# Performance work log

Hardware: AMD Instinct MI355X
Metric: run time of the kernel (lower is better)

The kernel has to match this reference:

```python
import jax, jax.numpy as jnp
import numpy as np

N = 100000
E = 3200000
F_IN, H1, H2, C = 512, 32, 16, 11


def setup_inputs() -> dict:
    key = jax.random.key(0)
    ks = jax.random.split(key, 8)
    x = jax.random.normal(ks[0], (N, F_IN), dtype=jnp.float32)
    edge_index = jax.random.randint(ks[1], (2, E), 0, N, dtype=jnp.int64)
    def glorot(k, fan_in, fan_out):
        lim = np.sqrt(6.0 / (fan_in + fan_out)).astype(np.float32)
        return jax.random.uniform(k, (fan_in, fan_out), jnp.float32, -lim, lim)
    return {
        "x": x,
        "edge_index": edge_index,
        "W1": glorot(ks[2], F_IN, H1), "b1": jnp.zeros((H1,), jnp.float32),
        "W2": glorot(ks[3], H1, H2),   "b2": jnp.zeros((H2,), jnp.float32),
        "W3": glorot(ks[4], H2, C),    "b3": jnp.zeros((C,), jnp.float32),
    }


def _gcn_conv(x, W, b, src, dst, deg_inv_sqrt):
    # GCNConv: D^{-1/2}(A+I)D^{-1/2} X W + b, self-loops handled analytically.
    h = x @ W                                   # [N, out]
    norm = deg_inv_sqrt[src] * deg_inv_sqrt[dst]  # [E]
    msg = h[src] * norm[:, None]                # gather + scale
    agg = jax.ops.segment_sum(msg, dst, num_segments=x.shape[0])
    agg = agg + h * (deg_inv_sqrt ** 2)[:, None]  # self-loop term
    return agg + b


def reference(x, edge_index, W1, b1, W2, b2, W3, b3):
    src, dst = edge_index[0], edge_index[1]
    n = x.shape[0]
    # degree with self-loops, counted on destination (PyG convention)
    deg = jax.ops.segment_sum(jnp.ones((dst.shape[0],), x.dtype), dst, num_segments=n) + 1.0
    deg_inv_sqrt = jax.lax.rsqrt(deg)
    h = jax.nn.relu(_gcn_conv(x, W1, b1, src, dst, deg_inv_sqrt))
    # F.dropout(training=self.training) is identity in eval mode
    h = jax.nn.relu(_gcn_conv(h, W2, b2, src, dst, deg_inv_sqrt))
    h = _gcn_conv(h, W3, b3, src, dst, deg_inv_sqrt)
    return jax.nn.log_softmax(h, axis=1)
```

## Files before the change

### kernel.cpp

```cpp
#include <hip/hip_runtime.h>
#include <hip/hip_bf16.h>

static __device__ __forceinline__ unsigned short f2bf(float f) {
    unsigned u = __float_as_uint(f);
    unsigned r = (u + 0x7FFF + ((u >> 16) & 1)) >> 16;
    return (unsigned short)r;
}
static __device__ __forceinline__ float bf2f(unsigned short h) {
    return __uint_as_float(((unsigned)h) << 16);
}
static __device__ __forceinline__ float bflo(unsigned v) { return __uint_as_float(v << 16); }
static __device__ __forceinline__ float bfhi(unsigned v) { return __uint_as_float(v & 0xFFFF0000u); }
static __device__ __forceinline__ unsigned pack2bf(float a, float b) {
    __hip_bfloat162 h2 = __float22bfloat162_rn(float2{a, b});
    union { __hip_bfloat162 h; unsigned u; } cv;
    cv.h = h2;
    return cv.u;
}

typedef __attribute__((ext_vector_type(8))) short bf16x8;
typedef __attribute__((ext_vector_type(8))) unsigned short u16x8;
typedef __attribute__((ext_vector_type(4))) float f32x4;

#define BKT_SHIFT 7
#define BKT_NODES 128
#define CHUNK 16384

__global__ __launch_bounds__(512) void hist_k(const int* __restrict__ dst, int* __restrict__ histG,
                                              int B, int NB, int E) {
    __shared__ int hist[1024];
    int tid = threadIdx.x;
    for (int i = tid; i < NB; i += 512) hist[i] = 0;
    __syncthreads();
    int base = blockIdx.x * CHUNK;
    for (int i = tid; i < CHUNK; i += 512) {
        int e = base + i;
        if (e >= E) break;
        atomicAdd(&hist[dst[e] >> BKT_SHIFT], 1);
    }
    __syncthreads();
    for (int i = tid; i < NB; i += 512) histG[(size_t)i * B + blockIdx.x] = hist[i];
}

__global__ __launch_bounds__(512) void scatter_k(const int* __restrict__ src, const int* __restrict__ dst,
                                                 const int* __restrict__ scanG, const int* __restrict__ blksum,
                                                 int* __restrict__ pairs, int B, int NB, int E) {
    __shared__ int sbase[1024];
    __shared__ int scnt[1024];
    int tid = threadIdx.x;
    for (int i = tid; i < NB; i += 512) {
        size_t idx = (size_t)i * B + blockIdx.x;
        sbase[i] = scanG[idx] + blksum[idx >> 11];
        scnt[i] = 0;
    }
    __syncthreads();
    int base = blockIdx.x * CHUNK;
    for (int i = tid; i < CHUNK; i += 512) {
        int e = base + i;
        if (e >= E) break;
        int d = dst[e], s = src[e];
        int b = d >> BKT_SHIFT;
        int r = atomicAdd(&scnt[b], 1);
        pairs[sbase[b] + r] = (s << BKT_SHIFT) | (d & (BKT_NODES - 1));
    }
}

#define SCAN_VPT 8
#define SCAN_ELEMS 2048

__global__ __launch_bounds__(256) void scan1(const int* __restrict__ in, int* __restrict__ out,
                                             int* __restrict__ blksum, int n) {
    __shared__ int sh[256];
    int base = blockIdx.x * SCAN_ELEMS + threadIdx.x * SCAN_VPT;
    int v[SCAN_VPT];
    int sum = 0;
    #pragma unroll
    for (int j = 0; j < SCAN_VPT; ++j) {
        v[j] = (base + j < n) ? in[base + j] : 0;
        sum += v[j];
    }
    sh[threadIdx.x] = sum;
    __syncthreads();
    for (int off = 1; off < 256; off <<= 1) {
        int t = (threadIdx.x >= off) ? sh[threadIdx.x - off] : 0;
        __syncthreads();
        sh[threadIdx.x] += t;
        __syncthreads();
    }
    if (threadIdx.x == 255) blksum[blockIdx.x] = sh[255];
    int run = sh[threadIdx.x] - sum;
    #pragma unroll
    for (int j = 0; j < SCAN_VPT; ++j) {
        if (base + j < n) out[base + j] = run;
        run += v[j];
    }
}

__global__ __launch_bounds__(256) void scan2(int* __restrict__ blksum, int nb) {
    __shared__ int sh[256];
    int t = threadIdx.x;
    int v = (t < nb) ? blksum[t] : 0;
    sh[t] = v;
    __syncthreads();
    for (int off = 1; off < 256; off <<= 1) {
        int u = (t >= off) ? sh[t - off] : 0;
        __syncthreads();
        sh[t] += u;
        __syncthreads();
    }
    if (t < nb) blksum[t] = sh[t] - v;
}

__global__ __launch_bounds__(256) void wconv(const float* __restrict__ W, unsigned short* __restrict__ W1T) {
    int gidx = blockIdx.x * 256 + threadIdx.x;
    if (gidx < 32 * 512) {
        int c = gidx >> 9, k = gidx & 511;
        W1T[gidx] = f2bf(W[(size_t)k * 32 + c]);
    }
}

#define SORT_CAP 8192

__global__ __launch_bounds__(512) void sort_bucket(const int* __restrict__ pairs,
        const int* __restrict__ scanG, const int* __restrict__ blksum, int B, int NB,
        int* __restrict__ csr_src, int* __restrict__ node_start,
        int* __restrict__ cnt, float* __restrict__ dis, int n, int E) {
    __shared__ int keys[SORT_CAP];
    __shared__ int lcnt[BKT_NODES];
    __shared__ int lscan[BKT_NODES];
    __shared__ int lfill[BKT_NODES];
    int bkt = blockIdx.x, tid = threadIdx.x;
    size_t idx0 = (size_t)bkt * B;
    int e0 = scanG[idx0] + blksum[idx0 >> 11];
    int e1 = E;
    if (bkt + 1 < NB) {
        size_t idx1 = (size_t)(bkt + 1) * B;
        e1 = scanG[idx1] + blksum[idx1 >> 11];
    }
    int m = e1 - e0;
    if (tid < BKT_NODES) { lcnt[tid] = 0; lfill[tid] = 0; }
    __syncthreads();
    for (int i = tid; i < m; i += 512) {
        int k = pairs[e0 + i];
        if (i < SORT_CAP) keys[i] = k;
        atomicAdd(&lcnt[k & (BKT_NODES - 1)], 1);
    }
    __syncthreads();
    if (tid < 64) {
        int c0 = lcnt[2 * tid], c1 = lcnt[2 * tid + 1];
        int s = c0 + c1;
        #pragma unroll
        for (int off = 1; off < 64; off <<= 1) {
            int t = __shfl_up(s, off);
            if (tid >= off) s += t;
        }
        lscan[2 * tid]     = s - c1 - c0;
        lscan[2 * tid + 1] = s - c1;
    }
    __syncthreads();
    int nb0 = bkt << BKT_SHIFT;
    if (tid < BKT_NODES && nb0 + tid < n) {
        int deg = lcnt[tid];
        node_start[nb0 + tid] = e0 + lscan[tid];
        cnt[nb0 + tid] = deg;
        dis[nb0 + tid] = rsqrtf((float)deg + 1.0f);
    }
    for (int i = tid; i < m; i += 512) {
        int k = (i < SORT_CAP) ? keys[i] : pairs[e0 + i];
        int d = k & (BKT_NODES - 1);
        int pos = lscan[d] + atomicAdd(&lfill[d], 1);
        csr_src[e0 + pos] = k >> BKT_SHIFT;
    }
}


__global__ __launch_bounds__(256) void gemm1_mfma(const float* __restrict__ x, const unsigned short* __restrict__ W1T,
                                                  const float* __restrict__ dis, unsigned short* __restrict__ g, int n) {
    __shared__ __attribute__((aligned(16))) unsigned short wT[32][520];
    __shared__ __attribute__((aligned(16))) unsigned short xb[64][72];
    int tid = threadIdx.x;
    int node0 = blockIdx.x * 64;

    #pragma unroll
    for (int r = 0; r < 8; ++r) {
        int u8 = tid + r * 256;
        int c = u8 >> 6, kq = (u8 & 63) * 8;
        *(u16x8*)(&wT[c][kq]) = *(const u16x8*)(W1T + (size_t)c * 512 + kq);
    }

    int wv_ = tid >> 6;
    int lane = tid & 63;
    int mrow = lane & 15;
    int kg = lane >> 4;
    f32x4 acc0 = {0.f, 0.f, 0.f, 0.f};
    f32x4 acc1 = {0.f, 0.f, 0.f, 0.f};

    for (int k0 = 0; k0 < 512; k0 += 64) {
        __syncthreads();
        #pragma unroll
        for (int r = 0; r < 4; ++r) {
            int fi = tid + r * 256;
            int nd = fi >> 4, kq = (fi & 15) * 4;
            int gn = min(node0 + nd, n - 1);
            float4 xv = *(const float4*)(x + (size_t)gn * 512 + k0 + kq);
            uint2 pw;
            pw.x = pack2bf(xv.x, xv.y);
            pw.y = pack2bf(xv.z, xv.w);
            *(uint2*)(&xb[nd][kq]) = pw;
        }
        __syncthreads();
        #pragma unroll
        for (int ks = 0; ks < 2; ++ks) {
            bf16x8 a  = *(const bf16x8*)(&xb[wv_ * 16 + mrow][ks * 32 + kg * 8]);
            bf16x8 b0 = *(const bf16x8*)(&wT[mrow][k0 + ks * 32 + kg * 8]);
            bf16x8 b1 = *(const bf16x8*)(&wT[16 + mrow][k0 + ks * 32 + kg * 8]);
            acc0 = __builtin_amdgcn_mfma_f32_16x16x32_bf16(a, b0, acc0, 0, 0, 0);
            acc1 = __builtin_amdgcn_mfma_f32_16x16x32_bf16(a, b1, acc1, 0, 0, 0);
        }
    }
    #pragma unroll
    for (int j = 0; j < 4; ++j) {
        int node = node0 + wv_ * 16 + kg * 4 + j;
        if (node < n) {
            float dv = dis[node];
            g[(size_t)node * 32 + mrow]      = f2bf(acc0[j] * dv);
            g[(size_t)node * 32 + 16 + mrow] = f2bf(acc1[j] * dv);
        }
    }
}


__global__ __launch_bounds__(256) void gather1(const int* __restrict__ csr_src,
        const int* __restrict__ start, const int* __restrict__ cnt,
        const unsigned short* __restrict__ g1, const float* __restrict__ dis,
        const float* __restrict__ b1, const float* __restrict__ W2,
        unsigned short* __restrict__ g2, int n) {
    __shared__ float w2s[32 * 16];
    for (int i = threadIdx.x; i < 512; i += 256) w2s[i] = W2[i];
    __syncthreads();
    int node = blockIdx.x * 4 + (threadIdx.x >> 6);
    if (node >= n) return;
    int lane = threadIdx.x & 63;
    int fpair = lane & 15;
    int j = lane >> 4;
    int i0 = start[node], i1 = i0 + cnt[node];
    float alo = 0.f, ahi = 0.f;
    int i = i0 + j;
    for (; i + 12 < i1; i += 16) {
        int s1 = csr_src[i];
        int s2 = csr_src[i + 4];
        int s3 = csr_src[i + 8];
        int s4 = csr_src[i + 12];
        unsigned v1 = *(const unsigned*)(g1 + (size_t)s1 * 32 + fpair * 2);
        unsigned v2 = *(const unsigned*)(g1 + (size_t)s2 * 32 + fpair * 2);
        unsigned v3 = *(const unsigned*)(g1 + (size_t)s3 * 32 + fpair * 2);
        unsigned v4 = *(const unsigned*)(g1 + (size_t)s4 * 32 + fpair * 2);
        alo += bflo(v1) + bflo(v2) + bflo(v3) + bflo(v4);
        ahi += bfhi(v1) + bfhi(v2) + bfhi(v3) + bfhi(v4);
    }
    for (; i < i1; i += 4) {
        unsigned v = *(const unsigned*)(g1 + (size_t)csr_src[i] * 32 + fpair * 2);
        alo += bflo(v); ahi += bfhi(v);
    }
    alo += __shfl_xor(alo, 16); alo += __shfl_xor(alo, 32);
    ahi += __shfl_xor(ahi, 16); ahi += __shfl_xor(ahi, 32);
    float dv = dis[node];
    unsigned sv = *(const unsigned*)(g1 + (size_t)node * 32 + fpair * 2);
    float vlo = fmaxf((alo + bflo(sv)) * dv + b1[2 * fpair], 0.f);
    float vhi = fmaxf((ahi + bfhi(sv)) * dv + b1[2 * fpair + 1], 0.f);
    int c = fpair;
    float p = 0.f;
    #pragma unroll
    for (int qq = 0; qq < 4; ++qq) {
        int q = j * 4 + qq;
        float xlo = __shfl(vlo, q);
        float xhi = __shfl(vhi, q);
        p = fmaf(xlo, w2s[(2 * q) * 16 + c], p);
        p = fmaf(xhi, w2s[(2 * q + 1) * 16 + c], p);
    }
    p += __shfl_xor(p, 16);
    p += __shfl_xor(p, 32);
    if (lane < 16) g2[(size_t)node * 16 + c] = f2bf(p * dv);
}


__global__ __launch_bounds__(256) void gather2(const int* __restrict__ csr_src,
        const int* __restrict__ start, const int* __restrict__ cnt,
        const unsigned short* __restrict__ g2, const float* __restrict__ dis,
        const float* __restrict__ b2, const float* __restrict__ W3,
        unsigned short* __restrict__ g3, int n) {
    __shared__ float w3s[16 * 16];
    if (threadIdx.x < 256) {
        int k = threadIdx.x >> 4, c = threadIdx.x & 15;
        w3s[threadIdx.x] = (c < 11) ? W3[(size_t)k * 11 + c] : 0.f;
    }
    __syncthreads();
    int node = blockIdx.x * 4 + (threadIdx.x >> 6);
    if (node >= n) return;
    int lane = threadIdx.x & 63;
    int fpair = lane & 7;
    int j = lane >> 3;
    int i0 = start[node], i1 = i0 + cnt[node];
    float alo = 0.f, ahi = 0.f;
    int i = i0 + j;
    for (; i + 24 < i1; i += 32) {
        int s1 = csr_src[i];
        int s2 = csr_src[i + 8];
        int s3 = csr_src[i + 16];
        int s4 = csr_src[i + 24];
        unsigned v1 = *(const unsigned*)(g2 + (size_t)s1 * 16 + fpair * 2);
        unsigned v2 = *(const unsigned*)(g2 + (size_t)s2 * 16 + fpair * 2);
        unsigned v3 = *(const unsigned*)(g2 + (size_t)s3 * 16 + fpair * 2);
        unsigned v4 = *(const unsigned*)(g2 + (size_t)s4 * 16 + fpair * 2);
        alo += bflo(v1) + bflo(v2) + bflo(v3) + bflo(v4);
        ahi += bfhi(v1) + bfhi(v2) + bfhi(v3) + bfhi(v4);
    }
    for (; i < i1; i += 8) {
        unsigned v = *(const unsigned*)(g2 + (size_t)csr_src[i] * 16 + fpair * 2);
        alo += bflo(v); ahi += bfhi(v);
    }
    alo += __shfl_xor(alo, 8); alo += __shfl_xor(alo, 16); alo += __shfl_xor(alo, 32);
    ahi += __shfl_xor(ahi, 8); ahi += __shfl_xor(ahi, 16); ahi += __shfl_xor(ahi, 32);
    float dv = dis[node];
    unsigned sv = *(const unsigned*)(g2 + (size_t)node * 16 + fpair * 2);
    float vlo = fmaxf((alo + bflo(sv)) * dv + b2[2 * fpair], 0.f);
    float vhi = fmaxf((ahi + bfhi(sv)) * dv + b2[2 * fpair + 1], 0.f);
    int c = lane & 15;
    int j2 = lane >> 4;
    float p = 0.f;
    #pragma unroll
    for (int kk = 0; kk < 4; ++kk) {
        int k = j2 * 4 + kk;
        float xk = (kk & 1) ? __shfl(vhi, k >> 1) : __shfl(vlo, k >> 1);
        p = fmaf(xk, w3s[k * 16 + c], p);
    }
    p += __shfl_xor(p, 16);
    p += __shfl_xor(p, 32);
    if (lane < 16) g3[(size_t)node * 16 + c] = f2bf(p * dv);
}


__global__ __launch_bounds__(256) void gather3(const int* __restrict__ csr_src,
        const int* __restrict__ start, const int* __restrict__ cnt,
        const unsigned short* __restrict__ g, const float* __restrict__ dis,
        const float* __restrict__ bias, float* __restrict__ out, int n) {
    int node = blockIdx.x * 4 + (threadIdx.x >> 6);
    if (node >= n) return;
    int lane = threadIdx.x & 63;
    int fpair = lane & 7;
    int j = lane >> 3;
    int i0 = start[node], i1 = i0 + cnt[node];
    float alo = 0.f, ahi = 0.f;
    int i = i0 + j;
    for (; i + 24 < i1; i += 32) {
        int s1 = csr_src[i];
        int s2 = csr_src[i + 8];
        int s3 = csr_src[i + 16];
        int s4 = csr_src[i + 24];
        unsigned v1 = *(const unsigned*)(g + (size_t)s1 * 16 + fpair * 2);
        unsigned v2 = *(const unsigned*)(g + (size_t)s2 * 16 + fpair * 2);
        unsigned v3 = *(const unsigned*)(g + (size_t)s3 * 16 + fpair * 2);
        unsigned v4 = *(const unsigned*)(g + (size_t)s4 * 16 + fpair * 2);
        alo += bflo(v1) + bflo(v2) + bflo(v3) + bflo(v4);
        ahi += bfhi(v1) + bfhi(v2) + bfhi(v3) + bfhi(v4);
    }
    for (; i < i1; i += 8) {
        unsigned v = *(const unsigned*)(g + (size_t)csr_src[i] * 16 + fpair * 2);
        alo += bflo(v); ahi += bfhi(v);
    }
    alo += __shfl_xor(alo, 8); alo += __shfl_xor(alo, 16); alo += __shfl_xor(alo, 32);
    ahi += __shfl_xor(ahi, 8); ahi += __shfl_xor(ahi, 16); ahi += __shfl_xor(ahi, 32);
    unsigned sv = *(const unsigned*)(g + (size_t)node * 16 + fpair * 2);
    float dvn = dis[node];
    int flo = 2 * fpair, fhi = 2 * fpair + 1;
    bool oklo = flo < 11, okhi = fhi < 11;
    float vlo = (alo + bflo(sv)) * dvn + (oklo ? bias[flo] : 0.f);
    float vhi = (ahi + bfhi(sv)) * dvn + (okhi ? bias[fhi] : 0.f);
    float m = fmaxf(oklo ? vlo : -3.0e38f, okhi ? vhi : -3.0e38f);
    m = fmaxf(m, __shfl_xor(m, 1));
    m = fmaxf(m, __shfl_xor(m, 2));
    m = fmaxf(m, __shfl_xor(m, 4));
    float s = (oklo ? __expf(vlo - m) : 0.f) + (okhi ? __expf(vhi - m) : 0.f);
    s += __shfl_xor(s, 1); s += __shfl_xor(s, 2); s += __shfl_xor(s, 4);
    float ls = __logf(s) + m;
    if (lane < 8) {
        if (oklo) out[(size_t)node * 11 + flo] = vlo - ls;
        if (okhi) out[(size_t)node * 11 + fhi] = vhi - ls;
    }
}


extern "C" void kernel_launch(void* const* d_in, const int* in_sizes, int n_in,
                              void* d_out, int out_size, void* d_ws, size_t ws_size,
                              hipStream_t stream) {
    const float* x  = (const float*)d_in[0];
    const int*   ei = (const int*)d_in[1];
    const float* W1 = (const float*)d_in[2];
    const float* b1 = (const float*)d_in[3];
    const float* W2 = (const float*)d_in[4];
    const float* b2 = (const float*)d_in[5];
    const float* W3 = (const float*)d_in[6];
    const float* b3 = (const float*)d_in[7];
    float* out = (float*)d_out;

    const int n = in_sizes[0] / 512;
    const int E = in_sizes[1] / 2;
    const int* src = ei;
    const int* dst = ei + E;

    const int NB = (n + BKT_NODES - 1) >> BKT_SHIFT;
    const int B  = (E + CHUNK - 1) / CHUNK;
    const int NBB = NB * B;
    const int nb_scan = (NBB + SCAN_ELEMS - 1) / SCAN_ELEMS;

    int* ws0 = (int*)d_ws;
    size_t off = 0;
    int*   cnt     = ws0 + off; off += (size_t)n;
    float* dis     = (float*)(ws0 + off); off += (size_t)n;
    int*   nstart  = ws0 + off; off += (size_t)n;
    int*   scanG   = ws0 + off; off += (size_t)NBB;
    int*   blksum  = ws0 + off; off += 256;
    int*   pairs   = ws0 + off; off += (size_t)E;
    int*   csr_src = ws0 + off; off += (size_t)E;
    unsigned short* g1 = (unsigned short*)(ws0 + off); off += (size_t)n * 16;
    unsigned short* g2 = (unsigned short*)(ws0 + off); off += (size_t)n * 8;
    unsigned short* g3 = (unsigned short*)(ws0 + off); off += (size_t)n * 8;
    unsigned short* W1T = (unsigned short*)(ws0 + off); off += 8192;
    int*   histG   = (int*)g1;

    hist_k<<<B, 512, 0, stream>>>(dst, histG, B, NB, E);
    scan1<<<nb_scan, 256, 0, stream>>>(histG, scanG, blksum, NBB);
    scan2<<<1, 256, 0, stream>>>(blksum, nb_scan);
    wconv<<<64, 256, 0, stream>>>(W1, W1T);
    scatter_k<<<B, 512, 0, stream>>>(src, dst, scanG, blksum, pairs, B, NB, E);
    sort_bucket<<<NB, 512, 0, stream>>>(pairs, scanG, blksum, B, NB, csr_src, nstart, cnt, dis, n, E);

    gemm1_mfma<<<(n + 63) / 64, 256, 0, stream>>>(x, W1T, dis, g1, n);
    gather1<<<(n + 3) / 4, 256, 0, stream>>>(csr_src, nstart, cnt, g1, dis, b1, W2, g2, n);
    gather2<<<(n + 3) / 4, 256, 0, stream>>>(csr_src, nstart, cnt, g2, dis, b2, W3, g3, n);
    gather3<<<(n + 3) / 4, 256, 0, stream>>>(csr_src, nstart, cnt, g3, dis, b3, out, n);
}
```

Baseline: 291.0 us.

## Load x directly into MFMA registers and widen gather loads to 8 bytes

The first-layer GEMM stops staging x through shared memory. Each lane now loads its own row slice as two float4 values, converts them to bf16 in registers and feeds the MFMA directly, which removes the per-k-tile __syncthreads pairs and LDS traffic. All three gather kernels switch from 4-byte to 8-byte (uint2) loads per lane, with four accumulators each, so more edges are processed per lane group. The small weight tables are stored transposed and padded in shared memory for the dense epilogue. The direct x loads are less coalesced across the wave, since each lane reads a 32-byte slice of a different row.

New measurement: 286.1 us. About the same (-1.7%).

```diff
diff --git a/kernel.cpp b/kernel.cpp
--- a/kernel.cpp
+++ b/kernel.cpp
@@ -5,9 +5,6 @@
     unsigned u = __float_as_uint(f);
     unsigned r = (u + 0x7FFF + ((u >> 16) & 1)) >> 16;
     return (unsigned short)r;
-}
-static __device__ __forceinline__ float bf2f(unsigned short h) {
-    return __uint_as_float(((unsigned)h) << 16);
 }
 static __device__ __forceinline__ float bflo(unsigned v) { return __uint_as_float(v << 16); }
 static __device__ __forceinline__ float bfhi(unsigned v) { return __uint_as_float(v & 0xFFFF0000u); }
@@ -177,7 +174,6 @@
 __global__ __launch_bounds__(256) void gemm1_mfma(const float* __restrict__ x, const unsigned short* __restrict__ W1T,
                                                   const float* __restrict__ dis, unsigned short* __restrict__ g, int n) {
     __shared__ __attribute__((aligned(16))) unsigned short wT[32][520];
-    __shared__ __attribute__((aligned(16))) unsigned short xb[64][72];
     int tid = threadIdx.x;
     int node0 = blockIdx.x * 64;
 
@@ -192,31 +188,26 @@
     int lane = tid & 63;
     int mrow = lane & 15;
     int kg = lane >> 4;
+    int lnode = node0 + wv_ * 16 + mrow;
+    int gn = min(lnode, n - 1);
+    const float* xrow = x + (size_t)gn * 512 + kg * 8;
     f32x4 acc0 = {0.f, 0.f, 0.f, 0.f};
     f32x4 acc1 = {0.f, 0.f, 0.f, 0.f};
-
-    for (int k0 = 0; k0 < 512; k0 += 64) {
-        __syncthreads();
-        #pragma unroll
-        for (int r = 0; r < 4; ++r) {
-            int fi = tid + r * 256;
-            int nd = fi >> 4, kq = (fi & 15) * 4;
-            int gn = min(node0 + nd, n - 1);
-            float4 xv = *(const float4*)(x + (size_t)gn * 512 + k0 + kq);
-            uint2 pw;
-            pw.x = pack2bf(xv.x, xv.y);
-            pw.y = pack2bf(xv.z, xv.w);
-            *(uint2*)(&xb[nd][kq]) = pw;
-        }
-        __syncthreads();
-        #pragma unroll
-        for (int ks = 0; ks < 2; ++ks) {
-            bf16x8 a  = *(const bf16x8*)(&xb[wv_ * 16 + mrow][ks * 32 + kg * 8]);
-            bf16x8 b0 = *(const bf16x8*)(&wT[mrow][k0 + ks * 32 + kg * 8]);
-            bf16x8 b1 = *(const bf16x8*)(&wT[16 + mrow][k0 + ks * 32 + kg * 8]);
-            acc0 = __builtin_amdgcn_mfma_f32_16x16x32_bf16(a, b0, acc0, 0, 0, 0);
-            acc1 = __builtin_amdgcn_mfma_f32_16x16x32_bf16(a, b1, acc1, 0, 0, 0);
-        }
+    __syncthreads();
+
+    #pragma unroll 4
+    for (int k0 = 0; k0 < 512; k0 += 32) {
+        float4 xa = *(const float4*)(xrow + k0);
+        float4 xc = *(const float4*)(xrow + k0 + 4);
+        union { unsigned u[4]; bf16x8 v; } a;
+        a.u[0] = pack2bf(xa.x, xa.y);
+        a.u[1] = pack2bf(xa.z, xa.w);
+        a.u[2] = pack2bf(xc.x, xc.y);
+        a.u[3] = pack2bf(xc.z, xc.w);
+        bf16x8 b0 = *(const bf16x8*)(&wT[mrow][k0 + kg * 8]);
+        bf16x8 b1 = *(const bf16x8*)(&wT[16 + mrow][k0 + kg * 8]);
+        acc0 = __builtin_amdgcn_mfma_f32_16x16x32_bf16(a.v, b0, acc0, 0, 0, 0);
+        acc1 = __builtin_amdgcn_mfma_f32_16x16x32_bf16(a.v, b1, acc1, 0, 0, 0);
     }
     #pragma unroll
     for (int j = 0; j < 4; ++j) {
@@ -235,104 +226,127 @@
         const unsigned short* __restrict__ g1, const float* __restrict__ dis,
         const float* __restrict__ b1, const float* __restrict__ W2,
         unsigned short* __restrict__ g2, int n) {
-    __shared__ float w2s[32 * 16];
-    for (int i = threadIdx.x; i < 512; i += 256) w2s[i] = W2[i];
+    __shared__ float w2t[16 * 33];
+    for (int i = threadIdx.x; i < 512; i += 256) {
+        int k = i >> 4, c = i & 15;
+        w2t[c * 33 + k] = W2[i];
+    }
     __syncthreads();
     int node = blockIdx.x * 4 + (threadIdx.x >> 6);
     if (node >= n) return;
     int lane = threadIdx.x & 63;
-    int fpair = lane & 15;
-    int j = lane >> 4;
-    int i0 = start[node], i1 = i0 + cnt[node];
-    float alo = 0.f, ahi = 0.f;
-    int i = i0 + j;
-    for (; i + 12 < i1; i += 16) {
-        int s1 = csr_src[i];
-        int s2 = csr_src[i + 4];
-        int s3 = csr_src[i + 8];
-        int s4 = csr_src[i + 12];
-        unsigned v1 = *(const unsigned*)(g1 + (size_t)s1 * 32 + fpair * 2);
-        unsigned v2 = *(const unsigned*)(g1 + (size_t)s2 * 32 + fpair * 2);
-        unsigned v3 = *(const unsigned*)(g1 + (size_t)s3 * 32 + fpair * 2);
-        unsigned v4 = *(const unsigned*)(g1 + (size_t)s4 * 32 + fpair * 2);
-        alo += bflo(v1) + bflo(v2) + bflo(v3) + bflo(v4);
-        ahi += bfhi(v1) + bfhi(v2) + bfhi(v3) + bfhi(v4);
-    }
-    for (; i < i1; i += 4) {
-        unsigned v = *(const unsigned*)(g1 + (size_t)csr_src[i] * 32 + fpair * 2);
-        alo += bflo(v); ahi += bfhi(v);
-    }
-    alo += __shfl_xor(alo, 16); alo += __shfl_xor(alo, 32);
-    ahi += __shfl_xor(ahi, 16); ahi += __shfl_xor(ahi, 32);
-    float dv = dis[node];
-    unsigned sv = *(const unsigned*)(g1 + (size_t)node * 32 + fpair * 2);
-    float vlo = fmaxf((alo + bflo(sv)) * dv + b1[2 * fpair], 0.f);
-    float vhi = fmaxf((ahi + bfhi(sv)) * dv + b1[2 * fpair + 1], 0.f);
-    int c = fpair;
-    float p = 0.f;
-    #pragma unroll
-    for (int qq = 0; qq < 4; ++qq) {
-        int q = j * 4 + qq;
-        float xlo = __shfl(vlo, q);
-        float xhi = __shfl(vhi, q);
-        p = fmaf(xlo, w2s[(2 * q) * 16 + c], p);
-        p = fmaf(xhi, w2s[(2 * q + 1) * 16 + c], p);
-    }
-    p += __shfl_xor(p, 16);
-    p += __shfl_xor(p, 32);
-    if (lane < 16) g2[(size_t)node * 16 + c] = f2bf(p * dv);
-}
-
-
-__global__ __launch_bounds__(256) void gather2(const int* __restrict__ csr_src,
-        const int* __restrict__ start, const int* __restrict__ cnt,
-        const unsigned short* __restrict__ g2, const float* __restrict__ dis,
-        const float* __restrict__ b2, const float* __restrict__ W3,
-        unsigned short* __restrict__ g3, int n) {
-    __shared__ float w3s[16 * 16];
-    if (threadIdx.x < 256) {
-        int k = threadIdx.x >> 4, c = threadIdx.x & 15;
-        w3s[threadIdx.x] = (c < 11) ? W3[(size_t)k * 11 + c] : 0.f;
-    }
-    __syncthreads();
-    int node = blockIdx.x * 4 + (threadIdx.x >> 6);
-    if (node >= n) return;
-    int lane = threadIdx.x & 63;
-    int fpair = lane & 7;
+    int fq = lane & 7;
     int j = lane >> 3;
     int i0 = start[node], i1 = i0 + cnt[node];
-    float alo = 0.f, ahi = 0.f;
+    float a0 = 0.f, a1 = 0.f, a2 = 0.f, a3 = 0.f;
     int i = i0 + j;
     for (; i + 24 < i1; i += 32) {
         int s1 = csr_src[i];
         int s2 = csr_src[i + 8];
         int s3 = csr_src[i + 16];
         int s4 = csr_src[i + 24];
-        unsigned v1 = *(const unsigned*)(g2 + (size_t)s1 * 16 + fpair * 2);
-        unsigned v2 = *(const unsigned*)(g2 + (size_t)s2 * 16 + fpair * 2);
-        unsigned v3 = *(const unsigned*)(g2 + (size_t)s3 * 16 + fpair * 2);
-        unsigned v4 = *(const unsigned*)(g2 + (size_t)s4 * 16 + fpair * 2);
-        alo += bflo(v1) + bflo(v2) + bflo(v3) + bflo(v4);
-        ahi += bfhi(v1) + bfhi(v2) + bfhi(v3) + bfhi(v4);
+        uint2 v1 = *(const uint2*)(g1 + (size_t)s1 * 32 + fq * 4);
+        uint2 v2 = *(const uint2*)(g1 + (size_t)s2 * 32 + fq * 4);
+        uint2 v3 = *(const uint2*)(g1 + (size_t)s3 * 32 + fq * 4);
+        uint2 v4 = *(const uint2*)(g1 + (size_t)s4 * 32 + fq * 4);
+        a0 += bflo(v1.x) + bflo(v2.x) + bflo(v3.x) + bflo(v4.x);
+        a1 += bfhi(v1.x) + bfhi(v2.x) + bfhi(v3.x) + bfhi(v4.x);
+        a2 += bflo(v1.y) + bflo(v2.y) + bflo(v3.y) + bflo(v4.y);
+        a3 += bfhi(v1.y) + bfhi(v2.y) + bfhi(v3.y) + bfhi(v4.y);
     }
     for (; i < i1; i += 8) {
-        unsigned v = *(const unsigned*)(g2 + (size_t)csr_src[i] * 16 + fpair * 2);
-        alo += bflo(v); ahi += bfhi(v);
-    }
-    alo += __shfl_xor(alo, 8); alo += __shfl_xor(alo, 16); alo += __shfl_xor(alo, 32);
-    ahi += __shfl_xor(ahi, 8); ahi += __shfl_xor(ahi, 16); ahi += __shfl_xor(ahi, 32);
+        uint2 v = *(const uint2*)(g1 + (size_t)csr_src[i] * 32 + fq * 4);
+        a0 += bflo(v.x); a1 += bfhi(v.x);
+        a2 += bflo(v.y); a3 += bfhi(v.y);
+    }
+    #pragma unroll
+    for (int m = 8; m < 64; m <<= 1) {
+        a0 += __shfl_xor(a0, m); a1 += __shfl_xor(a1, m);
+        a2 += __shfl_xor(a2, m); a3 += __shfl_xor(a3, m);
+    }
     float dv = dis[node];
-    unsigned sv = *(const unsigned*)(g2 + (size_t)node * 16 + fpair * 2);
-    float vlo = fmaxf((alo + bflo(sv)) * dv + b2[2 * fpair], 0.f);
-    float vhi = fmaxf((ahi + bfhi(sv)) * dv + b2[2 * fpair + 1], 0.f);
+    uint2 sv = *(const uint2*)(g1 + (size_t)node * 32 + fq * 4);
+    float v0 = fmaxf((a0 + bflo(sv.x)) * dv + b1[4 * fq + 0], 0.f);
+    float v1f = fmaxf((a1 + bfhi(sv.x)) * dv + b1[4 * fq + 1], 0.f);
+    float v2f = fmaxf((a2 + bflo(sv.y)) * dv + b1[4 * fq + 2], 0.f);
+    float v3f = fmaxf((a3 + bfhi(sv.y)) * dv + b1[4 * fq + 3], 0.f);
+    int c = lane & 15;
+    int j3 = lane >> 4;
+    float p = 0.f;
+    #pragma unroll
+    for (int kk = 0; kk < 8; ++kk) {
+        int k = j3 * 8 + kk;
+        int srcl = k >> 2;
+        float xk;
+        if ((kk & 3) == 0) xk = __shfl(v0, srcl);
+        else if ((kk & 3) == 1) xk = __shfl(v1f, srcl);
+        else if ((kk & 3) == 2) xk = __shfl(v2f, srcl);
+        else xk = __shfl(v3f, srcl);
+        p = fmaf(xk, w2t[c * 33 + k], p);
+    }
+    p += __shfl_xor(p, 16);
+    p += __shfl_xor(p, 32);
+    if (lane < 16) g2[(size_t)node * 16 + c] = f2bf(p * dv);
+}
+
+
+__global__ __launch_bounds__(256) void gather2(const int* __restrict__ csr_src,
+        const int* __restrict__ start, const int* __restrict__ cnt,
+        const unsigned short* __restrict__ g2, const float* __restrict__ dis,
+        const float* __restrict__ b2, const float* __restrict__ W3,
+        unsigned short* __restrict__ g3, int n) {
+    __shared__ float w3t[16 * 17];
+    if (threadIdx.x < 256) {
+        int k = threadIdx.x >> 4, c = threadIdx.x & 15;
+        w3t[c * 17 + k] = (c < 11) ? W3[(size_t)k * 11 + c] : 0.f;
+    }
+    __syncthreads();
+    int node = blockIdx.x * 4 + (threadIdx.x >> 6);
+    if (node >= n) return;
+    int lane = threadIdx.x & 63;
+    int fq = lane & 3;
+    int j = lane >> 2;
+    int i0 = start[node], i1 = i0 + cnt[node];
+    float a0 = 0.f, a1 = 0.f, a2 = 0.f, a3 = 0.f;
+    int i = i0 + j;
+    for (; i + 16 < i1; i += 32) {
+        int s1 = csr_src[i];
+        int s2 = csr_src[i + 16];
+        uint2 v1 = *(const uint2*)(g2 + (size_t)s1 * 16 + fq * 4);
+        uint2 v2 = *(const uint2*)(g2 + (size_t)s2 * 16 + fq * 4);
+        a0 += bflo(v1.x) + bflo(v2.x);
+        a1 += bfhi(v1.x) + bfhi(v2.x);
+        a2 += bflo(v1.y) + bflo(v2.y);
+        a3 += bfhi(v1.y) + bfhi(v2.y);
+    }
+    if (i < i1) {
+        uint2 v = *(const uint2*)(g2 + (size_t)csr_src[i] * 16 + fq * 4);
+        a0 += bflo(v.x); a1 += bfhi(v.x);
+        a2 += bflo(v.y); a3 += bfhi(v.y);
+    }
+    #pragma unroll
+    for (int m = 4; m < 64; m <<= 1) {
+        a0 += __shfl_xor(a0, m); a1 += __shfl_xor(a1, m);
+        a2 += __shfl_xor(a2, m); a3 += __shfl_xor(a3, m);
+    }
+    float dv = dis[node];
+    uint2 sv = *(const uint2*)(g2 + (size_t)node * 16 + fq * 4);
+    float v0 = fmaxf((a0 + bflo(sv.x)) * dv + b2[4 * fq + 0], 0.f);
+    float v1f = fmaxf((a1 + bfhi(sv.x)) * dv + b2[4 * fq + 1], 0.f);
+    float v2f = fmaxf((a2 + bflo(sv.y)) * dv + b2[4 * fq + 2], 0.f);
+    float v3f = fmaxf((a3 + bfhi(sv.y)) * dv + b2[4 * fq + 3], 0.f);
     int c = lane & 15;
     int j2 = lane >> 4;
     float p = 0.f;
-    #pragma unroll
-    for (int kk = 0; kk < 4; ++kk) {
-        int k = j2 * 4 + kk;
-        float xk = (kk & 1) ? __shfl(vhi, k >> 1) : __shfl(vlo, k >> 1);
-        p = fmaf(xk, w3s[k * 16 + c], p);
+    {
+        float xk0 = __shfl(v0, j2);
+        float xk1 = __shfl(v1f, j2);
+        float xk2 = __shfl(v2f, j2);
+        float xk3 = __shfl(v3f, j2);
+        p = fmaf(xk0, w3t[c * 17 + j2 * 4 + 0], p);
+        p = fmaf(xk1, w3t[c * 17 + j2 * 4 + 1], p);
+        p = fmaf(xk2, w3t[c * 17 + j2 * 4 + 2], p);
+        p = fmaf(xk3, w3t[c * 17 + j2 * 4 + 3], p);
     }
     p += __shfl_xor(p, 16);
     p += __shfl_xor(p, 32);
@@ -347,45 +361,55 @@
     int node = blockIdx.x * 4 + (threadIdx.x >> 6);
     if (node >= n) return;
     int lane = threadIdx.x & 63;
-    int fpair = lane & 7;
-    int j = lane >> 3;
+    int fq = lane & 3;
+    int j = lane >> 2;
     int i0 = start[node], i1 = i0 + cnt[node];
-    float alo = 0.f, ahi = 0.f;
+    float a0 = 0.f, a1 = 0.f, a2 = 0.f, a3 = 0.f;
     int i = i0 + j;
-    for (; i + 24 < i1; i += 32) {
+    for (; i + 16 < i1; i += 32) {
         int s1 = csr_src[i];
-        int s2 = csr_src[i + 8];
-        int s3 = csr_src[i + 16];
-        int s4 = csr_src[i + 24];
-        unsigned v1 = *(const unsigned*)(g + (size_t)s1 * 16 + fpair * 2);
-        unsigned v2 = *(const unsigned*)(g + (size_t)s2 * 16 + fpair * 2);
-        unsigned v3 = *(const unsigned*)(g + (size_t)s3 * 16 + fpair * 2);
-        unsigned v4 = *(const unsigned*)(g + (size_t)s4 * 16 + fpair * 2);
-        alo += bflo(v1) + bflo(v2) + bflo(v3) + bflo(v4);
-        ahi += bfhi(v1) + bfhi(v2) + bfhi(v3) + bfhi(v4);
-    }
-    for (; i < i1; i += 8) {
-        unsigned v = *(const unsigned*)(g + (size_t)csr_src[i] * 16 + fpair * 2);
-        alo += bflo(v); ahi += bfhi(v);
-    }
-    alo += __shfl_xor(alo, 8); alo += __shfl_xor(alo, 16); alo += __shfl_xor(alo, 32);
-    ahi += __shfl_xor(ahi, 8); ahi += __shfl_xor(ahi, 16); ahi += __shfl_xor(ahi, 32);
-    unsigned sv = *(const unsigned*)(g + (size_t)node * 16 + fpair * 2);
+        int s2 = csr_src[i + 16];
+        uint2 v1 = *(const uint2*)(g + (size_t)s1 * 16 + fq * 4);
+        uint2 v2 = *(const uint2*)(g + (size_t)s2 * 16 + fq * 4);
+        a0 += bflo(v1.x) + bflo(v2.x);
+        a1 += bfhi(v1.x) + bfhi(v2.x);
+        a2 += bflo(v1.y) + bflo(v2.y);
+        a3 += bfhi(v1.y) + bfhi(v2.y);
+    }
+    if (i < i1) {
+        uint2 v = *(const uint2*)(g + (size_t)csr_src[i] * 16 + fq * 4);
+        a0 += bflo(v.x); a1 += bfhi(v.x);
+        a2 += bflo(v.y); a3 += bfhi(v.y);
+    }
+    #pragma unroll
+    for (int m = 4; m < 64; m <<= 1) {
+        a0 += __shfl_xor(a0, m); a1 += __shfl_xor(a1, m);
+        a2 += __shfl_xor(a2, m); a3 += __shfl_xor(a3, m);
+    }
     float dvn = dis[node];
-    int flo = 2 * fpair, fhi = 2 * fpair + 1;
-    bool oklo = flo < 11, okhi = fhi < 11;
-    float vlo = (alo + bflo(sv)) * dvn + (oklo ? bias[flo] : 0.f);
-    float vhi = (ahi + bfhi(sv)) * dvn + (okhi ? bias[fhi] : 0.f);
-    float m = fmaxf(oklo ? vlo : -3.0e38f, okhi ? vhi : -3.0e38f);
-    m = fmaxf(m, __shfl_xor(m, 1));
-    m = fmaxf(m, __shfl_xor(m, 2));
-    m = fmaxf(m, __shfl_xor(m, 4));
-    float s = (oklo ? __expf(vlo - m) : 0.f) + (okhi ? __expf(vhi - m) : 0.f);
-    s += __shfl_xor(s, 1); s += __shfl_xor(s, 2); s += __shfl_xor(s, 4);
-    float ls = __logf(s) + m;
-    if (lane < 8) {
-        if (oklo) out[(size_t)node * 11 + flo] = vlo - ls;
-        if (okhi) out[(size_t)node * 11 + fhi] = vhi - ls;
+    uint2 sv = *(const uint2*)(g + (size_t)node * 16 + fq * 4);
+    int f0 = 4 * fq;
+    bool ok0 = f0 + 0 < 11, ok1 = f0 + 1 < 11, ok2 = f0 + 2 < 11, ok3 = f0 + 3 < 11;
+    float v0 = (a0 + bflo(sv.x)) * dvn + (ok0 ? bias[f0 + 0] : 0.f);
+    float v1f = (a1 + bfhi(sv.x)) * dvn + (ok1 ? bias[f0 + 1] : 0.f);
+    float v2f = (a2 + bflo(sv.y)) * dvn + (ok2 ? bias[f0 + 2] : 0.f);
+    float v3f = (a3 + bfhi(sv.y)) * dvn + (ok3 ? bias[f0 + 3] : 0.f);
+    const float NEG = -3.0e38f;
+    float m0 = fmaxf(fmaxf(ok0 ? v0 : NEG, ok1 ? v1f : NEG),
+                     fmaxf(ok2 ? v2f : NEG, ok3 ? v3f : NEG));
+    m0 = fmaxf(m0, __shfl_xor(m0, 1));
+    m0 = fmaxf(m0, __shfl_xor(m0, 2));
+    float s = (ok0 ? __expf(v0 - m0) : 0.f) + (ok1 ? __expf(v1f - m0) : 0.f)
+            + (ok2 ? __expf(v2f - m0) : 0.f) + (ok3 ? __expf(v3f - m0) : 0.f);
+    s += __shfl_xor(s, 1);
+    s += __shfl_xor(s, 2);
+    float ls = __logf(s) + m0;
+    if (lane < 4) {
+        float* orow = out + (size_t)node * 11 + f0;
+        if (ok0) orow[0] = v0 - ls;
+        if (ok1) orow[1] = v1f - ls;
+        if (ok2) orow[2] = v2f - ls;
+        if (ok3) orow[3] = v3f - ls;
     }
 }
 
```
